# Optimization experiments

Hardware: AMD Instinct MI355X
Metric: run time of the kernel (lower is better)

The kernel has to match this reference:

```python
import jax, jax.numpy as jnp
import numpy as np

N, M, K, D, H, C = 100000, 10000, 32, 64, 8, 64


def setup_inputs() -> dict:
    key = jax.random.key(0)
    ks = jax.random.split(key, 7)
    x = jax.random.normal(ks[0], (N, D), dtype=jnp.float32)
    src_idx = jax.random.randint(ks[1], (M, K), 0, N)
    dst_idx = jax.random.randint(ks[2], (M,), 0, N)
    # Linear weights stored as [in, out] (y = x @ W), matching torch Linear math
    Wq = jax.random.normal(ks[3], (D, D), dtype=jnp.float32) / np.sqrt(D)
    Wk = jax.random.normal(ks[4], (D, D * H), dtype=jnp.float32) / np.sqrt(D)
    Wp1 = jax.random.normal(ks[5], (H, H), dtype=jnp.float32) / np.sqrt(H)
    Wp2 = jax.random.normal(ks[6], (H, C), dtype=jnp.float32) / np.sqrt(H)
    return {"x": x, "src_idx": src_idx, "dst_idx": dst_idx,
            "Wq": Wq, "Wk": Wk, "Wp1": Wp1, "Wp2": Wp2}


def reference(x, src_idx, dst_idx, Wq, Wk, Wp1, Wp2):
    # gather destination / source node features (irregular access)
    n_i = x[dst_idx] @ Wq                              # [M, D]
    n_j = (x[src_idx] @ Wk).reshape(M, K, H, D)        # [M, K, H, D]
    # multi-head QK pair score, scaled by sqrt(dim)
    pair = jnp.einsum('md,mkhd->mkh', n_i, n_j) / jnp.sqrt(jnp.asarray(D, x.dtype))
    # small MLP head (dropout in eval mode = identity)
    hidden = jax.nn.relu(pair @ Wp1)                   # [M, K, H]
    logits = (hidden @ Wp2).reshape(M * K, C)          # [M*K, C]
    return logits
```

## Files before the change

kernel.cpp:

```cpp
#include <hip/hip_runtime.h>


#define Mm 10000
#define Kk 32
#define Dd 64
#define Hh 8
#define Cc 64

constexpr int MB_ = 16;
constexpr int PAIRS = 8;
constexpr size_t WC_FLOATS = 64 * 512;
constexpr size_t WS_NEED = WC_FLOATS * sizeof(float);

__global__ __launch_bounds__(256) void wc_build(
    const float* __restrict__ Wq,
    const float* __restrict__ Wk,
    float* __restrict__ WC)
{
    __shared__ float wq_l[16][68];
    __shared__ float wk_l[64][68];

    const int t  = threadIdx.x;
    const int e0 = blockIdx.x * 16;
    const int h  = blockIdx.y;

    {
        int r = t >> 4, q = t & 15;
        float4 v = ((const float4*)Wq)[(e0 + r) * 16 + q];
        *(float4*)&wq_l[r][q * 4] = v;
    }
    #pragma unroll
    for (int p = 0; p < 4; ++p) {
        int task = p * 256 + t;
        int dp = task >> 4, q = task & 15;
        float4 v = ((const float4*)Wk)[(size_t)dp * 128 + h * 16 + q];
        *(float4*)&wk_l[dp][q * 4] = v;
    }
    __syncthreads();

    const int dp = t & 63;
    const int eq = t >> 6;

    float4 wr[16];
    #pragma unroll
    for (int d4 = 0; d4 < 16; ++d4) wr[d4] = *(const float4*)&wk_l[dp][d4 * 4];

    #pragma unroll
    for (int i = 0; i < 4; ++i) {
        const int er = eq * 4 + i;
        float acc = 0.f;
        #pragma unroll
        for (int d4 = 0; d4 < 16; ++d4) {
            float4 qv = *(const float4*)&wq_l[er][d4 * 4];
            acc = fmaf(qv.x, wr[d4].x, acc);
            acc = fmaf(qv.y, wr[d4].y, acc);
            acc = fmaf(qv.z, wr[d4].z, acc);
            acc = fmaf(qv.w, wr[d4].w, acc);
        }
        WC[(size_t)(e0 + er) * 512 + h * 64 + dp] = acc * 0.125f;
    }
}

__global__ __launch_bounds__(512) void disto_AB(
    const float* __restrict__ x,
    const int*   __restrict__ src_idx,
    const int*   __restrict__ dst_idx,
    const float* __restrict__ WC,
    const float* __restrict__ Wp1,
    const float* __restrict__ Wp2,
    float* __restrict__ out)
{
    __shared__ float xs[2][64][68];
    __shared__ float dstx[2][2][68];
    __shared__ float a_lds[2][8][68];
    __shared__ float wp2_l[512];
    __shared__ int   idx_l[MB_ * Kk];
    __shared__ int   didx_l[MB_];

    const int t  = threadIdx.x;
    const int m0 = blockIdx.x * MB_;

    idx_l[t] = src_idx[m0 * Kk + t];
    if (t < MB_) didx_l[t] = dst_idx[m0 + t];
    if (t < 128) ((float4*)wp2_l)[t] = ((const float4*)Wp2)[t];

    float wc[64];
    #pragma unroll
    for (int e = 0; e < 64; ++e) wc[e] = WC[(size_t)e * 512 + t];

    __syncthreads();

    #pragma unroll
    for (int p = 0; p < 2; ++p) {
        int task = p * 512 + t;
        int r = task >> 4, q = task & 15;
        float4 v = ((const float4*)x)[(size_t)idx_l[r] * 16 + q];
        *(float4*)&xs[0][r][q * 4] = v;
    }
    if (t < 32) {
        float4 v = ((const float4*)x)[(size_t)didx_l[t >> 4] * 16 + (t & 15)];
        *(float4*)&dstx[0][t >> 4][(t & 15) * 4] = v;
    }

    const int l = t & 63, w = t >> 6;
    const int ml_w = w >> 2, ch = w & 3;
    const int h_role = l & 7, k8 = l >> 3;
    float wp1r[8];
    #pragma unroll
    for (int j = 0; j < 8; ++j) wp1r[j] = Wp1[h_role * Hh + j];

    __syncthreads();

    const int hh = t >> 6, dp = t & 63;
    int cur = 0;

    for (int p = 0; p < PAIRS; ++p) {
        float4 nx0, nx1, nd;
        const bool havepf = (p + 1 < PAIRS);
        const int r0 = t >> 4, q0 = t & 15;
        const int r1 = 32 + (t >> 4);
        if (havepf) {
            const int base = (p + 1) * 64;
            nx0 = ((const float4*)x)[(size_t)idx_l[base + r0] * 16 + q0];
            nx1 = ((const float4*)x)[(size_t)idx_l[base + r1] * 16 + q0];
            if (t < 32)
                nd = ((const float4*)x)[(size_t)didx_l[(p + 1) * 2 + (t >> 4)] * 16 + (t & 15)];
        }

        #pragma unroll
        for (int ml = 0; ml < 2; ++ml) {
            float a0 = 0.f, a1 = 0.f;
            #pragma unroll
            for (int e4 = 0; e4 < 16; ++e4) {
                float4 xv = *(const float4*)&dstx[cur][ml][e4 * 4];
                a0 = fmaf(xv.x, wc[e4 * 4 + 0], a0);
                a1 = fmaf(xv.y, wc[e4 * 4 + 1], a1);
                a0 = fmaf(xv.z, wc[e4 * 4 + 2], a0);
                a1 = fmaf(xv.w, wc[e4 * 4 + 3], a1);
            }
            a_lds[ml][hh][dp] = a0 + a1;
        }
        __syncthreads();

        {
            float pair = 0.f;
            const float4* xr = (const float4*)xs[cur][ml_w * 32 + ch * 8 + k8];
            const float4* ar = (const float4*)a_lds[ml_w][h_role];
            #pragma unroll
            for (int d4 = 0; d4 < 16; ++d4) {
                float4 xv = xr[d4];
                float4 av = ar[d4];
                pair = fmaf(xv.x, av.x, pair);
                pair = fmaf(xv.y, av.y, pair);
                pair = fmaf(xv.z, av.z, pair);
                pair = fmaf(xv.w, av.w, pair);
            }
            float hid[8];
            #pragma unroll
            for (int j = 0; j < 8; ++j) hid[j] = pair * wp1r[j];
            #pragma unroll
            for (int s = 1; s < 8; s <<= 1) {
                #pragma unroll
                for (int j = 0; j < 8; ++j)
                    hid[j] += __shfl_xor(hid[j], s, 64);
            }
            #pragma unroll
            for (int j = 0; j < 8; ++j) hid[j] = fmaxf(hid[j], 0.f);

            float lg[8] = {0, 0, 0, 0, 0, 0, 0, 0};
            #pragma unroll
            for (int hp = 0; hp < 8; ++hp) {
                const float* wrow = &wp2_l[hp * Cc + h_role * 8];
                float4 wa = *(const float4*)wrow;
                float4 wb = *(const float4*)(wrow + 4);
                lg[0] = fmaf(hid[hp], wa.x, lg[0]);
                lg[1] = fmaf(hid[hp], wa.y, lg[1]);
                lg[2] = fmaf(hid[hp], wa.z, lg[2]);
                lg[3] = fmaf(hid[hp], wa.w, lg[3]);
                lg[4] = fmaf(hid[hp], wb.x, lg[4]);
                lg[5] = fmaf(hid[hp], wb.y, lg[5]);
                lg[6] = fmaf(hid[hp], wb.z, lg[6]);
                lg[7] = fmaf(hid[hp], wb.w, lg[7]);
            }
            const int m = m0 + p * 2 + ml_w;
            size_t row = (size_t)m * Kk + ch * 8 + k8;
            float4* o4 = (float4*)(out + row * Cc + h_role * 8);
            o4[0] = make_float4(lg[0], lg[1], lg[2], lg[3]);
            o4[1] = make_float4(lg[4], lg[5], lg[6], lg[7]);
        }

        if (havepf) {
            const int nxt = cur ^ 1;
            *(float4*)&xs[nxt][r0][q0 * 4] = nx0;
            *(float4*)&xs[nxt][r1][q0 * 4] = nx1;
            if (t < 32)
                *(float4*)&dstx[nxt][t >> 4][(t & 15) * 4] = nd;
        }
        __syncthreads();
        cur ^= 1;
    }
}

constexpr int WAVES = 4;
constexpr int PAD = 68;

__global__ __launch_bounds__(256) void disto_fused(
    const float* __restrict__ x,
    const int*   __restrict__ src_idx,
    const int*   __restrict__ dst_idx,
    const float* __restrict__ Wq,
    const float* __restrict__ Wk,
    const float* __restrict__ Wp1,
    const float* __restrict__ Wp2,
    float* __restrict__ out)
{
    __shared__ float ni_lds[WAVES][Dd];
    __shared__ float A_lds[WAVES][Hh][PAD];
    __shared__ float xs_lds[WAVES][8][PAD];
    __shared__ float wp2_lds[Hh * Cc];

    const int t = threadIdx.x;
    const int w = t >> 6;
    const int l = t & 63;
    const int m = blockIdx.x * WAVES + w;

    if (t < 128) ((float4*)wp2_lds)[t] = ((const float4*)Wp2)[t];

    const int dst = dst_idx[m];
    float xd = x[(size_t)dst * Dd + l];
    float acc1 = 0.f;
    #pragma unroll
    for (int dp = 0; dp < Dd; ++dp) {
        float xv = __shfl(xd, dp, 64);
        acc1 = fmaf(xv, Wq[dp * Dd + l], acc1);
    }
    ni_lds[w][l] = acc1;
    __syncthreads();
    {
        const float4* ni4 = (const float4*)ni_lds[w];
        const float4* wkrow = (const float4*)(Wk + (size_t)l * (Dd * Hh));
        #pragma unroll
        for (int h = 0; h < Hh; ++h) {
            float a = 0.f;
            #pragma unroll
            for (int d4 = 0; d4 < Dd / 4; ++d4) {
                float4 nv = ni4[d4];
                float4 wv = wkrow[h * (Dd / 4) + d4];
                a = fmaf(nv.x, wv.x, a);
                a = fmaf(nv.y, wv.y, a);
                a = fmaf(nv.z, wv.z, a);
                a = fmaf(nv.w, wv.w, a);
            }
            A_lds[w][h][l] = a * 0.125f;
        }
    }
    const int h_role = l & 7;
    const int k8 = l >> 3;
    float wp1r[8];
    #pragma unroll
    for (int j = 0; j < 8; ++j) wp1r[j] = Wp1[h_role * Hh + j];
    __syncthreads();

    for (int kc = 0; kc < 4; ++kc) {
        #pragma unroll
        for (int p = 0; p < 2; ++p) {
            int task = p * 64 + l;
            int r = task >> 4;
            int jq = task & 15;
            int idx = src_idx[m * Kk + kc * 8 + r];
            float4 v = ((const float4*)x)[(size_t)idx * (Dd / 4) + jq];
            *(float4*)&xs_lds[w][r][jq * 4] = v;
        }
        __syncthreads();
        float pair = 0.f;
        {
            const float4* xsr = (const float4*)xs_lds[w][k8];
            const float4* ar  = (const float4*)A_lds[w][h_role];
            #pragma unroll
            for (int d4 = 0; d4 < Dd / 4; ++d4) {
                float4 xv = xsr[d4];
                float4 av = ar[d4];
                pair = fmaf(xv.x, av.x, pair);
                pair = fmaf(xv.y, av.y, pair);
                pair = fmaf(xv.z, av.z, pair);
                pair = fmaf(xv.w, av.w, pair);
            }
        }
        float hid[8];
        #pragma unroll
        for (int j = 0; j < 8; ++j) hid[j] = pair * wp1r[j];
        #pragma unroll
        for (int s = 1; s < 8; s <<= 1) {
            #pragma unroll
            for (int j = 0; j < 8; ++j)
                hid[j] += __shfl_xor(hid[j], s, 64);
        }
        #pragma unroll
        for (int j = 0; j < 8; ++j) hid[j] = fmaxf(hid[j], 0.f);
        float lg[8] = {0,0,0,0,0,0,0,0};
        #pragma unroll
        for (int hp = 0; hp < 8; ++hp) {
            const float* wrow = &wp2_lds[hp * Cc + h_role * 8];
            float4 wa = *(const float4*)wrow;
            float4 wb = *(const float4*)(wrow + 4);
            lg[0] = fmaf(hid[hp], wa.x, lg[0]);
            lg[1] = fmaf(hid[hp], wa.y, lg[1]);
            lg[2] = fmaf(hid[hp], wa.z, lg[2]);
            lg[3] = fmaf(hid[hp], wa.w, lg[3]);
            lg[4] = fmaf(hid[hp], wb.x, lg[4]);
            lg[5] = fmaf(hid[hp], wb.y, lg[5]);
            lg[6] = fmaf(hid[hp], wb.z, lg[6]);
            lg[7] = fmaf(hid[hp], wb.w, lg[7]);
        }
        size_t row = (size_t)(m * Kk + kc * 8 + k8);
        float4* o4 = (float4*)(out + row * Cc + h_role * 8);
        o4[0] = make_float4(lg[0], lg[1], lg[2], lg[3]);
        o4[1] = make_float4(lg[4], lg[5], lg[6], lg[7]);
        __syncthreads();
    }
}

extern "C" void kernel_launch(void* const* d_in, const int* in_sizes, int n_in,
                              void* d_out, int out_size, void* d_ws, size_t ws_size,
                              hipStream_t stream) {
    const float* x       = (const float*)d_in[0];
    const int*   src_idx = (const int*)  d_in[1];
    const int*   dst_idx = (const int*)  d_in[2];
    const float* Wq      = (const float*)d_in[3];
    const float* Wk      = (const float*)d_in[4];
    const float* Wp1     = (const float*)d_in[5];
    const float* Wp2     = (const float*)d_in[6];
    float* out = (float*)d_out;

    if (ws_size >= WS_NEED) {
        float* WC = (float*)d_ws;
        wc_build<<<dim3(4, 8), dim3(256), 0, stream>>>(Wq, Wk, WC);
        disto_AB<<<dim3(Mm / MB_), dim3(512), 0, stream>>>(
            x, src_idx, dst_idx, WC, Wp1, Wp2, out);
    } else {
        disto_fused<<<dim3(Mm / WAVES), dim3(256), 0, stream>>>(
            x, src_idx, dst_idx, Wq, Wk, Wp1, Wp2, out);
    }
}
```

Baseline: 160.4 us.

## Restructure disto_AB: precompute all dst projections, read source rows directly from global

Drops the double-buffered LDS staging of gathered source rows and the per-pair barriers. All 16 destination projections are computed up front into LDS. The main loop then reads source rows straight from global memory, and Wp2 is held in registers instead of LDS, which removes most __syncthreads and frees shared memory for higher occupancy via launch_bounds(512,4). The cost is that the gathered rows are no longer prefetched, so each of the 8 lanes sharing a source row issues a redundant global load and latency hiding depends on occupancy. Register pressure also rises.

```diff
diff --git a/kernel.cpp b/kernel.cpp
--- a/kernel.cpp
+++ b/kernel.cpp
@@ -8,7 +8,6 @@
 #define Cc 64
 
 constexpr int MB_ = 16;
-constexpr int PAIRS = 8;
 constexpr size_t WC_FLOATS = 64 * 512;
 constexpr size_t WS_NEED = WC_FLOATS * sizeof(float);
 
@@ -61,7 +60,7 @@
     }
 }
 
-__global__ __launch_bounds__(512) void disto_AB(
+__global__ __launch_bounds__(512, 4) void disto_AB(
     const float* __restrict__ x,
     const int*   __restrict__ src_idx,
     const int*   __restrict__ dst_idx,
@@ -70,134 +69,98 @@
     const float* __restrict__ Wp2,
     float* __restrict__ out)
 {
-    __shared__ float xs[2][64][68];
-    __shared__ float dstx[2][2][68];
-    __shared__ float a_lds[2][8][68];
-    __shared__ float wp2_l[512];
+    __shared__ float a_all[MB_][Hh][68];
+    __shared__ float dstx[MB_][68];
     __shared__ int   idx_l[MB_ * Kk];
-    __shared__ int   didx_l[MB_];
 
     const int t  = threadIdx.x;
     const int m0 = blockIdx.x * MB_;
 
     idx_l[t] = src_idx[m0 * Kk + t];
-    if (t < MB_) didx_l[t] = dst_idx[m0 + t];
-    if (t < 128) ((float4*)wp2_l)[t] = ((const float4*)Wp2)[t];
-
+    if (t < 256) {
+        int r = t >> 4, q = t & 15;
+        float4 v = ((const float4*)x)[(size_t)dst_idx[m0 + r] * 16 + q];
+        *(float4*)&dstx[r][q * 4] = v;
+    }
     float wc[64];
     #pragma unroll
     for (int e = 0; e < 64; ++e) wc[e] = WC[(size_t)e * 512 + t];
 
     __syncthreads();
 
-    #pragma unroll
-    for (int p = 0; p < 2; ++p) {
-        int task = p * 512 + t;
-        int r = task >> 4, q = task & 15;
-        float4 v = ((const float4*)x)[(size_t)idx_l[r] * 16 + q];
-        *(float4*)&xs[0][r][q * 4] = v;
-    }
-    if (t < 32) {
-        float4 v = ((const float4*)x)[(size_t)didx_l[t >> 4] * 16 + (t & 15)];
-        *(float4*)&dstx[0][t >> 4][(t & 15) * 4] = v;
-    }
-
-    const int l = t & 63, w = t >> 6;
+    const int hh = t >> 6, dp = t & 63;
+    for (int ml = 0; ml < MB_; ++ml) {
+        float a0 = 0.f, a1 = 0.f;
+        #pragma unroll
+        for (int e4 = 0; e4 < 16; ++e4) {
+            float4 xv = *(const float4*)&dstx[ml][e4 * 4];
+            a0 = fmaf(xv.x, wc[e4 * 4 + 0], a0);
+            a1 = fmaf(xv.y, wc[e4 * 4 + 1], a1);
+            a0 = fmaf(xv.z, wc[e4 * 4 + 2], a0);
+            a1 = fmaf(xv.w, wc[e4 * 4 + 3], a1);
+        }
+        a_all[ml][hh][dp] = a0 + a1;
+    }
+    __syncthreads();
+
+    const int w = t >> 6, l = t & 63;
     const int ml_w = w >> 2, ch = w & 3;
     const int h_role = l & 7, k8 = l >> 3;
+
     float wp1r[8];
     #pragma unroll
     for (int j = 0; j < 8; ++j) wp1r[j] = Wp1[h_role * Hh + j];
 
-    __syncthreads();
-
-    const int hh = t >> 6, dp = t & 63;
-    int cur = 0;
-
-    for (int p = 0; p < PAIRS; ++p) {
-        float4 nx0, nx1, nd;
-        const bool havepf = (p + 1 < PAIRS);
-        const int r0 = t >> 4, q0 = t & 15;
-        const int r1 = 32 + (t >> 4);
-        if (havepf) {
-            const int base = (p + 1) * 64;
-            nx0 = ((const float4*)x)[(size_t)idx_l[base + r0] * 16 + q0];
-            nx1 = ((const float4*)x)[(size_t)idx_l[base + r1] * 16 + q0];
-            if (t < 32)
-                nd = ((const float4*)x)[(size_t)didx_l[(p + 1) * 2 + (t >> 4)] * 16 + (t & 15)];
-        }
-
-        #pragma unroll
-        for (int ml = 0; ml < 2; ++ml) {
-            float a0 = 0.f, a1 = 0.f;
-            #pragma unroll
-            for (int e4 = 0; e4 < 16; ++e4) {
-                float4 xv = *(const float4*)&dstx[cur][ml][e4 * 4];
-                a0 = fmaf(xv.x, wc[e4 * 4 + 0], a0);
-                a1 = fmaf(xv.y, wc[e4 * 4 + 1], a1);
-                a0 = fmaf(xv.z, wc[e4 * 4 + 2], a0);
-                a1 = fmaf(xv.w, wc[e4 * 4 + 3], a1);
-            }
-            a_lds[ml][hh][dp] = a0 + a1;
-        }
-        __syncthreads();
-
-        {
-            float pair = 0.f;
-            const float4* xr = (const float4*)xs[cur][ml_w * 32 + ch * 8 + k8];
-            const float4* ar = (const float4*)a_lds[ml_w][h_role];
-            #pragma unroll
-            for (int d4 = 0; d4 < 16; ++d4) {
-                float4 xv = xr[d4];
-                float4 av = ar[d4];
-                pair = fmaf(xv.x, av.x, pair);
-                pair = fmaf(xv.y, av.y, pair);
-                pair = fmaf(xv.z, av.z, pair);
-                pair = fmaf(xv.w, av.w, pair);
-            }
-            float hid[8];
-            #pragma unroll
-            for (int j = 0; j < 8; ++j) hid[j] = pair * wp1r[j];
-            #pragma unroll
-            for (int s = 1; s < 8; s <<= 1) {
-                #pragma unroll
-                for (int j = 0; j < 8; ++j)
-                    hid[j] += __shfl_xor(hid[j], s, 64);
-            }
-            #pragma unroll
-            for (int j = 0; j < 8; ++j) hid[j] = fmaxf(hid[j], 0.f);
-
-            float lg[8] = {0, 0, 0, 0, 0, 0, 0, 0};
-            #pragma unroll
-            for (int hp = 0; hp < 8; ++hp) {
-                const float* wrow = &wp2_l[hp * Cc + h_role * 8];
-                float4 wa = *(const float4*)wrow;
-                float4 wb = *(const float4*)(wrow + 4);
-                lg[0] = fmaf(hid[hp], wa.x, lg[0]);
-                lg[1] = fmaf(hid[hp], wa.y, lg[1]);
-                lg[2] = fmaf(hid[hp], wa.z, lg[2]);
-                lg[3] = fmaf(hid[hp], wa.w, lg[3]);
-                lg[4] = fmaf(hid[hp], wb.x, lg[4]);
-                lg[5] = fmaf(hid[hp], wb.y, lg[5]);
-                lg[6] = fmaf(hid[hp], wb.z, lg[6]);
-                lg[7] = fmaf(hid[hp], wb.w, lg[7]);
-            }
-            const int m = m0 + p * 2 + ml_w;
-            size_t row = (size_t)m * Kk + ch * 8 + k8;
-            float4* o4 = (float4*)(out + row * Cc + h_role * 8);
-            o4[0] = make_float4(lg[0], lg[1], lg[2], lg[3]);
-            o4[1] = make_float4(lg[4], lg[5], lg[6], lg[7]);
-        }
-
-        if (havepf) {
-            const int nxt = cur ^ 1;
-            *(float4*)&xs[nxt][r0][q0 * 4] = nx0;
-            *(float4*)&xs[nxt][r1][q0 * 4] = nx1;
-            if (t < 32)
-                *(float4*)&dstx[nxt][t >> 4][(t & 15) * 4] = nd;
-        }
-        __syncthreads();
-        cur ^= 1;
+    float wp2r[8][8];
+    #pragma unroll
+    for (int hp = 0; hp < 8; ++hp) {
+        float4 wa = ((const float4*)Wp2)[hp * 16 + h_role * 2];
+        float4 wb = ((const float4*)Wp2)[hp * 16 + h_role * 2 + 1];
+        wp2r[hp][0] = wa.x; wp2r[hp][1] = wa.y; wp2r[hp][2] = wa.z; wp2r[hp][3] = wa.w;
+        wp2r[hp][4] = wb.x; wp2r[hp][5] = wb.y; wp2r[hp][6] = wb.z; wp2r[hp][7] = wb.w;
+    }
+
+    for (int p = 0; p < 8; ++p) {
+        const int mloc = p * 2 + ml_w;
+        const int ridx = idx_l[mloc * Kk + ch * 8 + k8];
+        const float4* xr = (const float4*)(x + (size_t)ridx * Dd);
+        const float4* ar = (const float4*)a_all[mloc][h_role];
+
+        float p0 = 0.f, p1 = 0.f;
+        #pragma unroll
+        for (int d4 = 0; d4 < 16; d4 += 2) {
+            float4 xv0 = xr[d4],     av0 = ar[d4];
+            float4 xv1 = xr[d4 + 1], av1 = ar[d4 + 1];
+            p0 = fmaf(xv0.x, av0.x, p0); p1 = fmaf(xv1.x, av1.x, p1);
+            p0 = fmaf(xv0.y, av0.y, p0); p1 = fmaf(xv1.y, av1.y, p1);
+            p0 = fmaf(xv0.z, av0.z, p0); p1 = fmaf(xv1.z, av1.z, p1);
+            p0 = fmaf(xv0.w, av0.w, p0); p1 = fmaf(xv1.w, av1.w, p1);
+        }
+        const float pair = p0 + p1;
+
+        float hid[8];
+        #pragma unroll
+        for (int j = 0; j < 8; ++j) hid[j] = pair * wp1r[j];
+        #pragma unroll
+        for (int s = 1; s < 8; s <<= 1) {
+            #pragma unroll
+            for (int j = 0; j < 8; ++j)
+                hid[j] += __shfl_xor(hid[j], s, 64);
+        }
+        #pragma unroll
+        for (int j = 0; j < 8; ++j) hid[j] = fmaxf(hid[j], 0.f);
+
+        float lg[8] = {0, 0, 0, 0, 0, 0, 0, 0};
+        #pragma unroll
+        for (int hp = 0; hp < 8; ++hp) {
+            #pragma unroll
+            for (int cc = 0; cc < 8; ++cc)
+                lg[cc] = fmaf(hid[hp], wp2r[hp][cc], lg[cc]);
+        }
+        size_t row = (size_t)(m0 + mloc) * Kk + ch * 8 + k8;
+        float4* o4 = (float4*)(out + row * Cc + h_role * 8);
+        o4[0] = make_float4(lg[0], lg[1], lg[2], lg[3]);
+        o4[1] = make_float4(lg[4], lg[5], lg[6], lg[7]);
     }
 }
 
```

New measurement: 238.9 us. +48.9%, slower.
